# Kernel tuning notes

Hardware: AMD Instinct MI355X
Metric: run time of the kernel (lower is better)

Reference implementation:

```python
import jax, jax.numpy as jnp
import numpy as np

N_NODES = 100000
N_EDGES = 1600000
D_IN = 128
D_OUT = 128


def setup_inputs() -> dict:
    key = jax.random.key(0)
    k1, k2, k3, k4, k5, k6 = jax.random.split(key, 6)
    x = jax.random.normal(k1, (N_NODES, D_IN), dtype=jnp.float32)
    edge_src = jax.random.randint(k2, (N_EDGES,), 0, N_NODES, dtype=jnp.int64 if jax.config.jax_enable_x64 else jnp.int32)
    edge_dst = jax.random.randint(k3, (N_EDGES,), 0, N_NODES, dtype=jnp.int64 if jax.config.jax_enable_x64 else jnp.int32)
    edge_val = jax.random.uniform(k4, (N_EDGES,), dtype=jnp.float32)
    # nn.Linear(2*D_IN, D_OUT): store W as [2*D_IN, D_OUT] (transposed torch layout)
    W = jax.random.normal(k5, (2 * D_IN, D_OUT), dtype=jnp.float32) * (1.0 / np.sqrt(2 * D_IN))
    b = jax.random.normal(k6, (D_OUT,), dtype=jnp.float32) * 0.01
    return {"x": x, "edge_src": edge_src, "edge_dst": edge_dst, "edge_val": edge_val, "W": W, "b": b}


def reference(x, edge_src, edge_dst, edge_val, W, b):
    # support = adj @ x  (sparse COO: adj[dst, src] = edge_val)
    gathered = x[edge_src] * edge_val[:, None]               # [E, D_IN]
    support = jax.ops.segment_sum(gathered, edge_dst, num_segments=x.shape[0])  # [N, D_IN]
    # concat self + aggregated neighbor features, then linear
    h = jnp.concatenate([x, support], axis=1)                # [N, 2*D_IN]
    return h @ W + b                                          # [N, D_OUT]
```

## Files before the change

kernel.cpp:

```cpp
#include <hip/hip_runtime.h>

#define D 128
#define BN 64
#define NBIN 391
#define NBMAX 512
#define CHUNK 4096
#define SCAP 12

typedef __attribute__((ext_vector_type(8))) short bf16x8;
typedef __attribute__((ext_vector_type(4))) float f32x4;

__device__ __forceinline__ unsigned short f2bf(float f) {
    unsigned int u = __builtin_bit_cast(unsigned int, f);
    u = (u + 0x7fffu + ((u >> 16) & 1u)) >> 16;
    return (unsigned short)u;
}
__device__ __forceinline__ float bf2f(unsigned int u) {
    return __builtin_bit_cast(float, u << 16);
}

__global__ void prep_kernel(const float* __restrict__ x,
                            unsigned short* __restrict__ x_bf,
                            const float* __restrict__ W,
                            unsigned short* __restrict__ WT,
                            int n4, int XB) {
    int blk = blockIdx.x, tid = threadIdx.x;
    if (blk < XB) {
        int i = blk * 256 + tid;
        if (i < n4) {
            float4 v = ((const float4*)x)[i];
            ushort4 s;
            s.x = f2bf(v.x); s.y = f2bf(v.y); s.z = f2bf(v.z); s.w = f2bf(v.w);
            ((ushort4*)x_bf)[i] = s;
        }
    } else {
        int t = (blk - XB) * 256 + tid;
        if (t < 2 * D * D) {
            int col = t & 127, k = t >> 7;
            WT[col * 256 + k] = f2bf(W[k * D + col]);
        }
    }
}

__global__ __launch_bounds__(512) void hist_kernel(const int* __restrict__ edst,
                                                   int* __restrict__ hcnt, int E) {
    __shared__ int h[NBMAX];
    const int t = threadIdx.x, c = blockIdx.x;
    h[t] = 0;
    __syncthreads();
    const int base = c * CHUNK;
    const int n = min(CHUNK, E - base);
#pragma unroll
    for (int k = 0; k < 8; ++k) {
        int li = k * 512 + t;
        if (li < n) atomicAdd(&h[edst[base + li] >> 8], 1);
    }
    __syncthreads();
    hcnt[c * NBMAX + t] = h[t];
}

__global__ __launch_bounds__(256) void binscan_kernel(const int* __restrict__ hcnt,
                                                      int* __restrict__ cpos,
                                                      int* __restrict__ ccnt, int NCH) {
    const int tid = threadIdx.x;
    const int lane = tid & 63;
    const int b = blockIdx.x * 4 + (tid >> 6);
    int run = 0;
    for (int c0 = 0; c0 < NCH; c0 += 64) {
        int c = c0 + lane;
        int v = (c < NCH) ? hcnt[c * NBMAX + b] : 0;
        int s = v;
#pragma unroll
        for (int off = 1; off < 64; off <<= 1) {
            int u = __shfl_up(s, off, 64);
            if (lane >= off) s += u;
        }
        if (c < NCH) cpos[b * NCH + c] = run + s - v;
        run += __shfl(s, 63, 64);
    }
    if (lane == 0) ccnt[b] = run;
}

__global__ __launch_bounds__(256) void cscan_kernel(const int* __restrict__ ccnt,
                                                    int* __restrict__ cbase) {
    __shared__ int p[256];
    int t = threadIdx.x;
    int s0 = ccnt[2 * t], s1 = ccnt[2 * t + 1];
    int loc = s0 + s1;
    p[t] = loc;
    __syncthreads();
    for (int off = 1; off < 256; off <<= 1) {
        int v = p[t];
        int u = (t >= off) ? p[t - off] : 0;
        __syncthreads();
        p[t] = v + u;
        __syncthreads();
    }
    int ex = p[t] - loc;
    cbase[2 * t] = ex;
    cbase[2 * t + 1] = ex + s0;
}

__global__ __launch_bounds__(512) void cfill_kernel(const int* __restrict__ esrc,
                                                    const int* __restrict__ edst,
                                                    const float* __restrict__ eval,
                                                    const int* __restrict__ cbase,
                                                    const int* __restrict__ cpos,
                                                    int2* __restrict__ ep, int E, int NCH) {
    __shared__ int lh[NBMAX];
    __shared__ int lcur[NBMAX];
    __shared__ int p[NBMAX];
    __shared__ int2 ord[CHUNK];
    __shared__ unsigned short obk[CHUNK];

    const int t = threadIdx.x;
    const int blk = blockIdx.x;
    const int base = blk * CHUNK;
    const int n = min(CHUNK, E - base);

    lh[t] = 0;
    __syncthreads();

    int esv[8]; int ebk[8];
    float evv[8];
#pragma unroll
    for (int k = 0; k < 8; ++k) {
        int li = k * 512 + t;
        if (li < n) {
            int i = base + li;
            int dst = edst[i];
            esv[k] = esrc[i];
            evv[k] = eval[i];
            int b = dst >> 8;
            ebk[k] = b | ((dst & 255) << 16);
            atomicAdd(&lh[b], 1);
        } else ebk[k] = -1;
    }
    __syncthreads();

    int cnt = lh[t];
    p[t] = cnt;
    __syncthreads();
    for (int off = 1; off < NBMAX; off <<= 1) {
        int v = p[t];
        int u = (t >= off) ? p[t - off] : 0;
        __syncthreads();
        p[t] = v + u;
        __syncthreads();
    }
    lcur[t] = p[t] - cnt;
    __syncthreads();

#pragma unroll
    for (int k = 0; k < 8; ++k) {
        if (ebk[k] >= 0) {
            int b = ebk[k] & 0xffff, nl = ebk[k] >> 16;
            int slot = atomicAdd(&lcur[b], 1);
            ord[slot] = make_int2((esv[k] << 8) | nl, __builtin_bit_cast(int, evv[k]));
            obk[slot] = (unsigned short)b;
        }
    }
    __syncthreads();

    if (t < NBIN) {
        int c2 = lh[t];
        if (c2) lh[t] = cbase[t] + cpos[t * NCH + blk] - (lcur[t] - c2);
    }
    __syncthreads();

    for (int i = t; i < n; i += 512) {
        int b = obk[i];
        ep[lh[b] + i] = ord[i];
    }
}

__global__ __launch_bounds__(512) void csort_kernel(int2* __restrict__ ep,
                                                    const int* __restrict__ cbase,
                                                    const int* __restrict__ ccnt,
                                                    int* __restrict__ node_start) {
    __shared__ int h[256];
    __shared__ int p[256];

    const int t = threadIdx.x;
    const int bin = blockIdx.x;
    const int cb = cbase[bin];
    const int ce = cb + ccnt[bin];

    if (t < 256) h[t] = 0;
    __syncthreads();

    int2 ev[SCAP];
#pragma unroll
    for (int k = 0; k < SCAP; ++k) {
        int idx = cb + k * 512 + t;
        if (idx < ce) {
            int2 e = ep[idx];
            ev[k] = e;
            atomicAdd(&h[e.x & 255], 1);
        } else ev[k] = make_int2(-1, 0);
    }
    __syncthreads();

    int c = 0;
    if (t < 256) { c = h[t]; p[t] = c; }
    __syncthreads();
    for (int off = 1; off < 256; off <<= 1) {
        int v = 0, u = 0;
        if (t < 256) { v = p[t]; u = (t >= off) ? p[t - off] : 0; }
        __syncthreads();
        if (t < 256) p[t] = v + u;
        __syncthreads();
    }
    if (t < 256) {
        int st = cb + p[t] - c;
        node_start[bin * 256 + t] = st;
        h[t] = st;
    }
    __syncthreads();

#pragma unroll
    for (int k = 0; k < SCAP; ++k) {
        if (ev[k].x >= 0) {
            int nl = ev[k].x & 255;
            int pos = atomicAdd(&h[nl], 1);
            ep[pos] = make_int2(ev[k].x & 0xFFFFFF3F, ev[k].y);
        }
    }
}

__global__ __launch_bounds__(256, 8) void gather_fused_kernel(
        const unsigned short* __restrict__ x_bf,
        const int* __restrict__ node_start,
        const int2* __restrict__ edge_pack,
        const unsigned short* __restrict__ WT,
        const float* __restrict__ bias,
        float* __restrict__ out, int N) {
    __shared__ unsigned short accb[BN * 136];
    __shared__ int nb[BN + 1];

    const int tid = threadIdx.x;
    const int node0 = blockIdx.x * BN;
    const int w = tid >> 6, lane = tid & 63;
    unsigned int* accw = (unsigned int*)accb;

    for (int i = tid * 8; i < BN * 136; i += 2048)
        *(uint4*)(accb + i) = make_uint4(0u, 0u, 0u, 0u);
    if (tid <= BN) nb[tid] = node_start[node0 + tid];
    __syncthreads();

    const int js = __builtin_amdgcn_readfirstlane(nb[w * 16]);
    const int je = __builtin_amdgcn_readfirstlane(nb[w * 16 + 16]);
    const unsigned short* xl = x_bf + lane * 2;

    int cur = -1;
    float ax = 0.f, ay = 0.f;
    for (int g = js; g < je; g += 16) {
        int m = je - g; if (m > 16) m = 16;
        int2 e[16];
#pragma unroll
        for (int k = 0; k < 16; ++k) {
            int idx = g + k; if (idx >= je) idx = je - 1;
            e[k] = edge_pack[idx];
        }
        unsigned int p[16];
#pragma unroll
        for (int k = 0; k < 16; ++k)
            p[k] = *(const unsigned int*)(xl + ((e[k].x >> 8) << 7));
#pragma unroll
        for (int k = 0; k < 16; ++k) {
            if (k < m) {
                int nd = e[k].x & 63;
                if (nd != cur) {
                    if (cur >= 0)
                        accw[cur * 68 + lane] =
                            (unsigned int)f2bf(ax) | ((unsigned int)f2bf(ay) << 16);
                    cur = nd; ax = 0.f; ay = 0.f;
                }
                float v = __builtin_bit_cast(float, e[k].y);
                ax += bf2f(p[k] & 0xffffu) * v;
                ay += bf2f(p[k] >> 16) * v;
            }
        }
    }
    if (cur >= 0)
        accw[cur * 68 + lane] = (unsigned int)f2bf(ax) | ((unsigned int)f2bf(ay) << 16);
    __syncthreads();

    const int quad = lane >> 4;
    const int l15  = lane & 15;
    const int colbase = w * 32;

    f32x4 acc[4][2];
#pragma unroll
    for (int rt = 0; rt < 4; ++rt) {
        acc[rt][0] = (f32x4){0.f, 0.f, 0.f, 0.f};
        acc[rt][1] = (f32x4){0.f, 0.f, 0.f, 0.f};
    }

#pragma unroll
    for (int ks = 0; ks < 8; ++ks) {
        bf16x8 wf0 = *(const bf16x8*)(WT + (size_t)(colbase + l15) * 256 + ks * 32 + quad * 8);
        bf16x8 wf1 = *(const bf16x8*)(WT + (size_t)(colbase + 16 + l15) * 256 + ks * 32 + quad * 8);
#pragma unroll
        for (int rt = 0; rt < 4; ++rt) {
            int row = rt * 16 + l15;
            bf16x8 a;
            if (ks < 4) {
                int rg = node0 + row; if (rg >= N) rg = N - 1;
                a = *(const bf16x8*)(x_bf + (size_t)rg * D + ks * 32 + quad * 8);
            } else {
                a = *(const bf16x8*)(accb + row * 136 + (ks - 4) * 32 + quad * 8);
            }
            acc[rt][0] = __builtin_amdgcn_mfma_f32_16x16x32_bf16(a, wf0, acc[rt][0], 0, 0, 0);
            acc[rt][1] = __builtin_amdgcn_mfma_f32_16x16x32_bf16(a, wf1, acc[rt][1], 0, 0, 0);
        }
    }

#pragma unroll
    for (int ct = 0; ct < 2; ++ct) {
        int col = colbase + ct * 16 + l15;
        float bv = bias[col];
#pragma unroll
        for (int rt = 0; rt < 4; ++rt) {
#pragma unroll
            for (int rg = 0; rg < 4; ++rg) {
                int row = node0 + rt * 16 + quad * 4 + rg;
                if (row < N)
                    out[(size_t)row * D + col] = acc[rt][ct][rg] + bv;
            }
        }
    }
}

extern "C" void kernel_launch(void* const* d_in, const int* in_sizes, int n_in,
                              void* d_out, int out_size, void* d_ws, size_t ws_size,
                              hipStream_t stream) {
    const float* x    = (const float*)d_in[0];
    const int*   esrc = (const int*)d_in[1];
    const int*   edst = (const int*)d_in[2];
    const float* eval = (const float*)d_in[3];
    const float* W    = (const float*)d_in[4];
    const float* bias = (const float*)d_in[5];
    float*       out  = (float*)d_out;

    const int N  = in_sizes[0] / D;
    const int E  = in_sizes[1];
    const int NG  = (N + BN - 1) / BN;
    const int NCH = (E + CHUNK - 1) / CHUNK;

    char* ws = (char*)d_ws;
    unsigned short* x_bf  = (unsigned short*)ws;
    int2*           ep    = (int2*)(ws + 25600000);
    int*            hcnt  = (int*)(ws + 25600000);
    unsigned short* WT    = (unsigned short*)(ws + 38400000);
    int*            nbg   = (int*)(ws + 38465536);
    int*            ccnt  = (int*)(ws + 38865920);
    int*            cbase = (int*)(ws + 38867968);
    int*            cpos  = (int*)(ws + 38870016);

    const int n4 = N * D / 4;
    const int XB = (n4 + 255) / 256;
    const int WB = (2 * D * D + 255) / 256;

    prep_kernel<<<XB + WB, 256, 0, stream>>>(x, x_bf, W, WT, n4, XB);
    hist_kernel<<<NCH, 512, 0, stream>>>(edst, hcnt, E);
    binscan_kernel<<<128, 256, 0, stream>>>(hcnt, cpos, ccnt, NCH);
    cscan_kernel<<<1, 256, 0, stream>>>(ccnt, cbase);
    cfill_kernel<<<NCH, 512, 0, stream>>>(esrc, edst, eval, cbase, cpos, ep, E, NCH);
    csort_kernel<<<NBIN, 512, 0, stream>>>(ep, cbase, ccnt, nbg);
    gather_fused_kernel<<<NG, 256, 0, stream>>>(x_bf, nbg, ep, WT, bias, out, N);
    (void)ws_size; (void)n_in; (void)out_size;
}
```

Baseline: 236.1 us.

## Fold histogram into prep kernel, drop cscan kernel, use wave-shuffle scans

Merges the destination-bin histogram into the prep launch as extra blocks and removes the single-block cscan launch. Each cfill and csort block now recomputes the bin base offsets with a wave-shuffle scan over ccnt. The serial shared-memory Hillis-Steele scans are replaced with two-level shuffle scans, and the hcnt/cpos layouts are transposed so the scan reads coalesced. This cuts two kernel launches and many block barriers, at the cost of redundant per-block scans of the bin counts.

```diff
diff --git a/kernel.cpp b/kernel.cpp
--- a/kernel.cpp
+++ b/kernel.cpp
@@ -23,7 +23,10 @@
                             unsigned short* __restrict__ x_bf,
                             const float* __restrict__ W,
                             unsigned short* __restrict__ WT,
-                            int n4, int XB) {
+                            const int* __restrict__ edst,
+                            int* __restrict__ hcnt,
+                            int n4, int XB, int WB, int E, int NCH) {
+    __shared__ int h[NBMAX];
     int blk = blockIdx.x, tid = threadIdx.x;
     if (blk < XB) {
         int i = blk * 256 + tid;
@@ -33,30 +36,27 @@
             s.x = f2bf(v.x); s.y = f2bf(v.y); s.z = f2bf(v.z); s.w = f2bf(v.w);
             ((ushort4*)x_bf)[i] = s;
         }
-    } else {
+    } else if (blk < XB + WB) {
         int t = (blk - XB) * 256 + tid;
         if (t < 2 * D * D) {
             int col = t & 127, k = t >> 7;
             WT[col * 256 + k] = f2bf(W[k * D + col]);
         }
-    }
-}
-
-__global__ __launch_bounds__(512) void hist_kernel(const int* __restrict__ edst,
-                                                   int* __restrict__ hcnt, int E) {
-    __shared__ int h[NBMAX];
-    const int t = threadIdx.x, c = blockIdx.x;
-    h[t] = 0;
-    __syncthreads();
-    const int base = c * CHUNK;
-    const int n = min(CHUNK, E - base);
-#pragma unroll
-    for (int k = 0; k < 8; ++k) {
-        int li = k * 512 + t;
-        if (li < n) atomicAdd(&h[edst[base + li] >> 8], 1);
-    }
-    __syncthreads();
-    hcnt[c * NBMAX + t] = h[t];
+    } else {
+        int c = blk - XB - WB;
+        h[tid] = 0; h[tid + 256] = 0;
+        __syncthreads();
+        int base = c * CHUNK;
+        int n = min(CHUNK, E - base);
+#pragma unroll
+        for (int k = 0; k < 16; ++k) {
+            int li = k * 256 + tid;
+            if (li < n) atomicAdd(&h[edst[base + li] >> 8], 1);
+        }
+        __syncthreads();
+        hcnt[tid * NCH + c]         = h[tid];
+        hcnt[(tid + 256) * NCH + c] = h[tid + 256];
+    }
 }
 
 __global__ __launch_bounds__(256) void binscan_kernel(const int* __restrict__ hcnt,
@@ -68,52 +68,34 @@
     int run = 0;
     for (int c0 = 0; c0 < NCH; c0 += 64) {
         int c = c0 + lane;
-        int v = (c < NCH) ? hcnt[c * NBMAX + b] : 0;
+        int v = (c < NCH) ? hcnt[b * NCH + c] : 0;
         int s = v;
 #pragma unroll
         for (int off = 1; off < 64; off <<= 1) {
             int u = __shfl_up(s, off, 64);
             if (lane >= off) s += u;
         }
-        if (c < NCH) cpos[b * NCH + c] = run + s - v;
+        if (c < NCH) cpos[c * NBMAX + b] = run + s - v;
         run += __shfl(s, 63, 64);
     }
     if (lane == 0) ccnt[b] = run;
-}
-
-__global__ __launch_bounds__(256) void cscan_kernel(const int* __restrict__ ccnt,
-                                                    int* __restrict__ cbase) {
-    __shared__ int p[256];
-    int t = threadIdx.x;
-    int s0 = ccnt[2 * t], s1 = ccnt[2 * t + 1];
-    int loc = s0 + s1;
-    p[t] = loc;
-    __syncthreads();
-    for (int off = 1; off < 256; off <<= 1) {
-        int v = p[t];
-        int u = (t >= off) ? p[t - off] : 0;
-        __syncthreads();
-        p[t] = v + u;
-        __syncthreads();
-    }
-    int ex = p[t] - loc;
-    cbase[2 * t] = ex;
-    cbase[2 * t + 1] = ex + s0;
 }
 
 __global__ __launch_bounds__(512) void cfill_kernel(const int* __restrict__ esrc,
                                                     const int* __restrict__ edst,
                                                     const float* __restrict__ eval,
-                                                    const int* __restrict__ cbase,
+                                                    const int* __restrict__ ccnt,
                                                     const int* __restrict__ cpos,
                                                     int2* __restrict__ ep, int E, int NCH) {
     __shared__ int lh[NBMAX];
     __shared__ int lcur[NBMAX];
-    __shared__ int p[NBMAX];
+    __shared__ int cbs[NBMAX];
+    __shared__ int wsum[16];
     __shared__ int2 ord[CHUNK];
     __shared__ unsigned short obk[CHUNK];
 
     const int t = threadIdx.x;
+    const int w = t >> 6, lane = t & 63;
     const int blk = blockIdx.x;
     const int base = blk * CHUNK;
     const int n = min(CHUNK, E - base);
@@ -138,17 +120,33 @@
     }
     __syncthreads();
 
-    int cnt = lh[t];
-    p[t] = cnt;
-    __syncthreads();
-    for (int off = 1; off < NBMAX; off <<= 1) {
-        int v = p[t];
-        int u = (t >= off) ? p[t - off] : 0;
-        __syncthreads();
-        p[t] = v + u;
-        __syncthreads();
-    }
-    lcur[t] = p[t] - cnt;
+    {
+        int v1 = lh[t], v2 = ccnt[t];
+        int s1 = v1, s2 = v2;
+#pragma unroll
+        for (int off = 1; off < 64; off <<= 1) {
+            int u1 = __shfl_up(s1, off, 64);
+            int u2 = __shfl_up(s2, off, 64);
+            if (lane >= off) { s1 += u1; s2 += u2; }
+        }
+        if (lane == 63) { wsum[w] = s1; wsum[8 + w] = s2; }
+        __syncthreads();
+        if (w == 0) {
+            int x1 = (lane < 8) ? wsum[lane] : 0;
+            int x2 = (lane < 8) ? wsum[8 + lane] : 0;
+            int y1 = x1, y2 = x2;
+#pragma unroll
+            for (int off = 1; off < 8; off <<= 1) {
+                int u1 = __shfl_up(y1, off, 64);
+                int u2 = __shfl_up(y2, off, 64);
+                if (lane >= off) { y1 += u1; y2 += u2; }
+            }
+            if (lane < 8) { wsum[lane] = y1 - x1; wsum[8 + lane] = y2 - x2; }
+        }
+        __syncthreads();
+        lcur[t] = s1 - v1 + wsum[w];
+        cbs[t]  = s2 - v2 + wsum[8 + w];
+    }
     __syncthreads();
 
 #pragma unroll
@@ -164,7 +162,7 @@
 
     if (t < NBIN) {
         int c2 = lh[t];
-        if (c2) lh[t] = cbase[t] + cpos[t * NCH + blk] - (lcur[t] - c2);
+        if (c2) lh[t] = cbs[t] + cpos[blk * NBMAX + t] - (lcur[t] - c2);
     }
     __syncthreads();
 
@@ -175,19 +173,44 @@
 }
 
 __global__ __launch_bounds__(512) void csort_kernel(int2* __restrict__ ep,
-                                                    const int* __restrict__ cbase,
                                                     const int* __restrict__ ccnt,
                                                     int* __restrict__ node_start) {
     __shared__ int h[256];
-    __shared__ int p[256];
+    __shared__ int cbs[NBMAX];
+    __shared__ int wsum[8];
 
     const int t = threadIdx.x;
+    const int w = t >> 6, lane = t & 63;
     const int bin = blockIdx.x;
-    const int cb = cbase[bin];
+
+    if (t < 256) h[t] = 0;
+    {
+        int v = ccnt[t];
+        int s = v;
+#pragma unroll
+        for (int off = 1; off < 64; off <<= 1) {
+            int u = __shfl_up(s, off, 64);
+            if (lane >= off) s += u;
+        }
+        if (lane == 63) wsum[w] = s;
+        __syncthreads();
+        if (w == 0) {
+            int x = (lane < 8) ? wsum[lane] : 0;
+            int y = x;
+#pragma unroll
+            for (int off = 1; off < 8; off <<= 1) {
+                int u = __shfl_up(y, off, 64);
+                if (lane >= off) y += u;
+            }
+            if (lane < 8) wsum[lane] = y - x;
+        }
+        __syncthreads();
+        cbs[t] = s - v + wsum[w];
+    }
+    __syncthreads();
+
+    const int cb = cbs[bin];
     const int ce = cb + ccnt[bin];
-
-    if (t < 256) h[t] = 0;
-    __syncthreads();
 
     int2 ev[SCAP];
 #pragma unroll
@@ -201,20 +224,32 @@
     }
     __syncthreads();
 
-    int c = 0;
-    if (t < 256) { c = h[t]; p[t] = c; }
-    __syncthreads();
-    for (int off = 1; off < 256; off <<= 1) {
-        int v = 0, u = 0;
-        if (t < 256) { v = p[t]; u = (t >= off) ? p[t - off] : 0; }
-        __syncthreads();
-        if (t < 256) p[t] = v + u;
-        __syncthreads();
-    }
-    if (t < 256) {
-        int st = cb + p[t] - c;
-        node_start[bin * 256 + t] = st;
-        h[t] = st;
+    {
+        int v = (t < 256) ? h[t] : 0;
+        int s = v;
+#pragma unroll
+        for (int off = 1; off < 64; off <<= 1) {
+            int u = __shfl_up(s, off, 64);
+            if (lane >= off) s += u;
+        }
+        if (lane == 63) wsum[w] = s;
+        __syncthreads();
+        if (w == 0) {
+            int x = (lane < 8) ? wsum[lane] : 0;
+            int y = x;
+#pragma unroll
+            for (int off = 1; off < 8; off <<= 1) {
+                int u = __shfl_up(y, off, 64);
+                if (lane >= off) y += u;
+            }
+            if (lane < 8) wsum[lane] = y - x;
+        }
+        __syncthreads();
+        if (t < 256) {
+            int st = cb + s - v + wsum[w];
+            node_start[bin * 256 + t] = st;
+            h[t] = st;
+        }
     }
     __syncthreads();
 
@@ -355,19 +390,17 @@
     unsigned short* WT    = (unsigned short*)(ws + 38400000);
     int*            nbg   = (int*)(ws + 38465536);
     int*            ccnt  = (int*)(ws + 38865920);
-    int*            cbase = (int*)(ws + 38867968);
     int*            cpos  = (int*)(ws + 38870016);
 
     const int n4 = N * D / 4;
     const int XB = (n4 + 255) / 256;
     const int WB = (2 * D * D + 255) / 256;
 
-    prep_kernel<<<XB + WB, 256, 0, stream>>>(x, x_bf, W, WT, n4, XB);
-    hist_kernel<<<NCH, 512, 0, stream>>>(edst, hcnt, E);
+    prep_kernel<<<XB + WB + NCH, 256, 0, stream>>>(x, x_bf, W, WT, edst, hcnt,
+                                                   n4, XB, WB, E, NCH);
     binscan_kernel<<<128, 256, 0, stream>>>(hcnt, cpos, ccnt, NCH);
-    cscan_kernel<<<1, 256, 0, stream>>>(ccnt, cbase);
-    cfill_kernel<<<NCH, 512, 0, stream>>>(esrc, edst, eval, cbase, cpos, ep, E, NCH);
-    csort_kernel<<<NBIN, 512, 0, stream>>>(ep, cbase, ccnt, nbg);
+    cfill_kernel<<<NCH, 512, 0, stream>>>(esrc, edst, eval, ccnt, cpos, ep, E, NCH);
+    csort_kernel<<<NBIN, 512, 0, stream>>>(ep, ccnt, nbg);
     gather_fused_kernel<<<NG, 256, 0, stream>>>(x_bf, nbg, ep, WT, bias, out, N);
     (void)ws_size; (void)n_in; (void)out_size;
 }
```

New measurement: 239.9 us. No clear change (+1.6%).
